# Kernel optimization log

Measured on AMD Instinct MI355X. Metric: run time of the kernel, lower is better.

The kernel has to match this reference:

```python
import jax, jax.numpy as jnp
import numpy as np

SEQ, BATCH, HIDDEN = 2048, 2, 1024
NUM_HEADS, HEAD_DIM = 16, 64
LN_EPS = 1e-6
NEG_INF = -1e10


def setup_inputs() -> dict:
    key = jax.random.key(0)
    k1, k2, k3 = jax.random.split(key, 3)
    inputs_q = jax.random.normal(k1, (SEQ, BATCH, HIDDEN), dtype=jnp.float32)
    ln_scale = jnp.ones((HIDDEN,), dtype=jnp.float32)
    ln_bias = jnp.zeros((HIDDEN,), dtype=jnp.float32)
    # fused QKV kernel: (hidden, 3, num_heads*head_dim), fan_in variance scaling
    qkv_kernel = jax.random.normal(k2, (HIDDEN, 3, NUM_HEADS * HEAD_DIM), dtype=jnp.float32) / np.sqrt(HIDDEN).astype(np.float32)
    out_kernel = jax.random.normal(k3, (NUM_HEADS * HEAD_DIM, HIDDEN), dtype=jnp.float32) / np.sqrt(NUM_HEADS * HEAD_DIM).astype(np.float32)
    return {"inputs_q": inputs_q, "ln_scale": ln_scale, "ln_bias": ln_bias,
            "qkv_kernel": qkv_kernel, "out_kernel": out_kernel}


def reference(inputs_q, ln_scale, ln_bias, qkv_kernel, out_kernel):
    s, b, h = inputs_q.shape
    # --- LayerNorm (fused with QKV projection in the original module) ---
    mu = jnp.mean(inputs_q, axis=-1, keepdims=True)
    var = jnp.mean(jnp.square(inputs_q - mu), axis=-1, keepdims=True)
    ln_out = (inputs_q - mu) * jax.lax.rsqrt(var + LN_EPS) * ln_scale + ln_bias
    # --- fused QKV projection: (s,b,h) @ (h,3,nh*hd) -> (s,b,3,nh*hd) ---
    qkv = jnp.einsum('sbh,htk->stbk', ln_out, qkv_kernel)  # (s,3,b,nh*hd)
    q = qkv[:, 0].reshape(s, b, NUM_HEADS, HEAD_DIM)  # (s,b,nh,hd)
    k = qkv[:, 1].reshape(s, b, NUM_HEADS, HEAD_DIM)
    v = qkv[:, 2].reshape(s, b, NUM_HEADS, HEAD_DIM)
    # --- core attention (transpose_batch_sequence=True layout) ---
    scale = 1.0 / np.sqrt(HEAD_DIM).astype(np.float32)  # scale_attn_logits=True
    logits = jnp.einsum('qbhd,kbhd->bhqk', q, k) * scale
    causal = jnp.tril(jnp.ones((s, s), dtype=bool))  # attn_mask_type='causal'
    logits = jnp.where(causal[None, None], logits, jnp.asarray(NEG_INF, logits.dtype))
    attn = jax.nn.softmax(logits, axis=-1)
    ctx = jnp.einsum('bhqk,kbhd->qbhd', attn, v).reshape(s, b, NUM_HEADS * HEAD_DIM)
    # --- output projection ---
    return jnp.einsum('sbk,kh->sbh', ctx, out_kernel)
```

## Files before the change

kernel.cpp:

```cpp
#include <hip/hip_runtime.h>

typedef unsigned short u16;
typedef unsigned int u32;
typedef __attribute__((ext_vector_type(8))) short short8;
typedef __attribute__((ext_vector_type(4))) float f32x4;

#define AS1C(p) ((const __attribute__((address_space(1))) void*)(p))
#define AS3(p)  ((__attribute__((address_space(3))) void*)(p))

constexpr int SEQ = 2048, BATCH = 2, HIDDEN = 1024, NH = 16, HD = 64;
constexpr int MROWS = SEQ * BATCH;
constexpr int QKV_N = 3 * NH * HD;
#define Q_SCALE 0.18033688011112042f

__device__ __forceinline__ float bf2f(u16 u) {
  union { u32 i; float f; } v; v.i = (u32)u << 16; return v.f;
}
__device__ __forceinline__ u16 f2bf(float f) {
  union { float f; u32 i; } v; v.f = f;
  u32 r = v.i + 0x7fffu + ((v.i >> 16) & 1u);
  return (u16)(r >> 16);
}
__device__ __forceinline__ u32 cvt_pk_bf16(float lo, float hi) {
  u32 r;
  asm("v_cvt_pk_bf16_f32 %0, %1, %2" : "=v"(r) : "v"(lo), "v"(hi));
  return r;
}
__device__ __forceinline__ bool is_f32(const unsigned* probe) { return probe[0] == 0x3F800000u; }

__global__ __launch_bounds__(256) void transpose_k(const void* __restrict__ in,
                                                   u16* __restrict__ out, int R, int C,
                                                   const unsigned* __restrict__ probe) {
  __shared__ alignas(16) u16 t[32][33];
  const bool fm = is_f32(probe);
  int c0 = blockIdx.x * 32, r0 = blockIdx.y * 32;
  int tx = threadIdx.x & 31, ty = threadIdx.x >> 5;
  if (fm) {
    const float* fin = (const float*)in;
#pragma unroll
    for (int i = 0; i < 32; i += 8) t[ty + i][tx] = f2bf(fin[(size_t)(r0 + ty + i) * C + c0 + tx]);
  } else {
    const u16* uin = (const u16*)in;
#pragma unroll
    for (int i = 0; i < 32; i += 8) t[ty + i][tx] = uin[(size_t)(r0 + ty + i) * C + c0 + tx];
  }
  __syncthreads();
#pragma unroll
  for (int i = 0; i < 32; i += 8) out[(size_t)(c0 + ty + i) * R + r0 + tx] = t[tx][ty + i];
}

__global__ __launch_bounds__(256) void ln_k(const void* __restrict__ xv, const void* __restrict__ gv,
                                            const void* __restrict__ bv, u16* __restrict__ y,
                                            const unsigned* __restrict__ probe) {
  const bool fm = is_f32(probe);
  int row = blockIdx.x, t = threadIdx.x;
  float f0, f1, f2, f3, g0, g1, g2, g3, b0, b1, b2, b3;
  if (fm) {
    float4 v = *(const float4*)((const float*)xv + (size_t)row * HIDDEN + t * 4);
    f0 = v.x; f1 = v.y; f2 = v.z; f3 = v.w;
    float4 gg = *(const float4*)((const float*)gv + t * 4);
    g0 = gg.x; g1 = gg.y; g2 = gg.z; g3 = gg.w;
    float4 bb = *(const float4*)((const float*)bv + t * 4);
    b0 = bb.x; b1 = bb.y; b2 = bb.z; b3 = bb.w;
  } else {
    ushort4 v = *(const ushort4*)((const u16*)xv + (size_t)row * HIDDEN + t * 4);
    f0 = bf2f(v.x); f1 = bf2f(v.y); f2 = bf2f(v.z); f3 = bf2f(v.w);
    ushort4 gg = *(const ushort4*)((const u16*)gv + t * 4);
    g0 = bf2f(gg.x); g1 = bf2f(gg.y); g2 = bf2f(gg.z); g3 = bf2f(gg.w);
    ushort4 bb = *(const ushort4*)((const u16*)bv + t * 4);
    b0 = bf2f(bb.x); b1 = bf2f(bb.y); b2 = bf2f(bb.z); b3 = bf2f(bb.w);
  }
  float s = f0 + f1 + f2 + f3;
  float s2 = f0 * f0 + f1 * f1 + f2 * f2 + f3 * f3;
#pragma unroll
  for (int off = 1; off < 64; off <<= 1) { s += __shfl_xor(s, off); s2 += __shfl_xor(s2, off); }
  __shared__ float ps[4], ps2[4];
  int w = t >> 6, lane = t & 63;
  if (lane == 0) { ps[w] = s; ps2[w] = s2; }
  __syncthreads();
  s = ps[0] + ps[1] + ps[2] + ps[3];
  s2 = ps2[0] + ps2[1] + ps2[2] + ps2[3];
  float mu = s * (1.0f / HIDDEN);
  float rstd = rsqrtf(s2 * (1.0f / HIDDEN) - mu * mu + 1e-6f);
  ushort4 o;
  o.x = f2bf((f0 - mu) * rstd * g0 + b0);
  o.y = f2bf((f1 - mu) * rstd * g1 + b1);
  o.z = f2bf((f2 - mu) * rstd * g2 + b2);
  o.w = f2bf((f3 - mu) * rstd * g3 + b3);
  *(ushort4*)(y + (size_t)row * HIDDEN + t * 4) = o;
}

template <int EPI>
__global__ __launch_bounds__(256) void gemm_k(const u16* __restrict__ A, const u16* __restrict__ Bt,
                                              void* __restrict__ o0, u16* __restrict__ o1,
                                              u16* __restrict__ o2, int M, int N, int K,
                                              const unsigned* __restrict__ probe) {
  __shared__ alignas(16) u16 As[128 * 32];
  __shared__ alignas(16) u16 Bs[128 * 32];
  const int bm = blockIdx.x, bn = blockIdx.y;
  const int tid = threadIdx.x, w = tid >> 6, lane = tid & 63;
  const int wr = w >> 1, wc = w & 1, lr = lane & 15, lk = lane >> 4;
  f32x4 acc[4][4] = {};

  const int srow_lo = lane >> 2;
  const int sslot = lane & 3;
  const int csw = ((lk ^ ((lr >> 1) & 3)) * 8);

  for (int k0 = 0; k0 < K; k0 += 32) {
#pragma unroll
    for (int j = 0; j < 2; j++) {
      const int issue = w * 2 + j;
      const int row = issue * 16 + srow_lo;
      const int src = ((sslot ^ ((row >> 1) & 3)) * 8);
      __builtin_amdgcn_global_load_lds(AS1C(A + (size_t)(bm * 128 + row) * K + k0 + src),
                                       AS3(As + issue * 512 + lane * 8), 16, 0, 0);
      __builtin_amdgcn_global_load_lds(AS1C(Bt + (size_t)(bn * 128 + row) * K + k0 + src),
                                       AS3(Bs + issue * 512 + lane * 8), 16, 0, 0);
    }
    __syncthreads();
    short8 a[4], b[4];
#pragma unroll
    for (int i = 0; i < 4; i++) {
      a[i] = *(const short8*)(As + (wr * 64 + i * 16 + lr) * 32 + csw);
      b[i] = *(const short8*)(Bs + (wc * 64 + i * 16 + lr) * 32 + csw);
    }
#pragma unroll
    for (int mi = 0; mi < 4; mi++)
#pragma unroll
      for (int ni = 0; ni < 4; ni++)
        acc[mi][ni] = __builtin_amdgcn_mfma_f32_16x16x32_bf16(a[mi], b[ni], acc[mi][ni], 0, 0, 0);
    __syncthreads();
  }

  const int r0 = bm * 128 + wr * 64, c0 = bn * 128 + wc * 64;
  if constexpr (EPI == 0) {
    const bool fm = is_f32(probe);
#pragma unroll
    for (int mi = 0; mi < 4; mi++)
#pragma unroll
      for (int ni = 0; ni < 4; ni++) {
        int col = c0 + ni * 16 + lr;
#pragma unroll
        for (int j = 0; j < 4; j++) {
          int row = r0 + mi * 16 + lk * 4 + j;
          if (fm) ((float*)o0)[(size_t)row * N + col] = acc[mi][ni][j];
          else    ((u16*)o0)[(size_t)row * N + col] = f2bf(acc[mi][ni][j]);
        }
      }
  } else {
#pragma unroll
    for (int mi = 0; mi < 4; mi++)
#pragma unroll
      for (int ni = 0; ni < 4; ni++) {
        int n = c0 + ni * 16 + lr;
        int t = n >> 10, rem = n & 1023, h = rem >> 6, d = rem & 63;
#pragma unroll
        for (int j = 0; j < 4; j++) {
          int r = r0 + mi * 16 + lk * 4 + j;
          int s = r >> 1, bb = r & 1;
          size_t bh = (size_t)(bb * NH + h);
          if (t == 0)      ((u16*)o0)[(bh * SEQ + s) * HD + d] = f2bf(acc[mi][ni][j] * Q_SCALE);
          else if (t == 1) o1[(bh * SEQ + s) * HD + d] = f2bf(acc[mi][ni][j]);
          else             o2[(bh * HD + d) * SEQ + s] = f2bf(acc[mi][ni][j]);
        }
      }
  }
}

__global__ __launch_bounds__(256, 3) void attn_k(const u16* __restrict__ Q, const u16* __restrict__ Kb,
                                                 const u16* __restrict__ VT, u16* __restrict__ ctx) {
  const int flat = blockIdx.x;
  const int xu = flat & 7, idx = flat >> 3;
  const int bh = xu * 4 + (idx & 3);
  const int qt = 31 - (idx >> 2);
  const int tid = threadIdx.x;
  const int w = tid >> 6, lane = tid & 63;
  const int lr = lane & 15, lk = lane >> 4;
  const size_t base = (size_t)bh * SEQ * HD;
  const int b = bh >> 4, h = bh & 15;

  __shared__ alignas(16) u16 Ks[2][4096];
  __shared__ alignas(16) u16 Vs[2][4096];
  __shared__ alignas(16) u16 P[4][16 * 72];
  u16* Pw = &P[w][0];
  u32* Pw32 = (u32*)Pw;

  const int st_r = lane >> 3;
  const int st_c = 8 * ((lane & 7) ^ st_r);

  const int qr0 = qt * 64 + w * 16;
  const int qrow = qr0 + lr;
  const int klast = qt;

  short8 aq[2];
#pragma unroll
  for (int kk = 0; kk < 2; kk++)
    aq[kk] = *(const short8*)(Q + base + (size_t)qrow * HD + kk * 32 + lk * 8);

  f32x4 o[4] = {};
  float m = -1e30f, l = 0.0f;

#pragma unroll
  for (int j = 0; j < 2; j++) {
    const int c = j * 4 + w;
    const int r = c * 8 + st_r;
    __builtin_amdgcn_global_load_lds(AS1C(Kb + base + (size_t)r * HD + st_c),
                                     AS3(Ks[0] + c * 512), 16, 0, 0);
    __builtin_amdgcn_global_load_lds(AS1C(VT + base + (size_t)r * SEQ + st_c),
                                     AS3(Vs[0] + c * 512), 16, 0, 0);
  }
  __syncthreads();

  for (int kt = 0; kt <= klast; kt++) {
    const int k0 = kt * 64;
    const int buf = kt & 1;
    if (kt < klast) {
      const int kn = k0 + 64;
#pragma unroll
      for (int j = 0; j < 2; j++) {
        const int c = j * 4 + w;
        const int r = c * 8 + st_r;
        __builtin_amdgcn_global_load_lds(AS1C(Kb + base + (size_t)(kn + r) * HD + st_c),
                                         AS3(Ks[buf ^ 1] + c * 512), 16, 0, 0);
        __builtin_amdgcn_global_load_lds(AS1C(VT + base + (size_t)r * SEQ + kn + st_c),
                                         AS3(Vs[buf ^ 1] + c * 512), 16, 0, 0);
      }
    }
    const int swz = (lr & 7) << 3;
    short8 bk[4][2], bv[4][2];
#pragma unroll
    for (int ni = 0; ni < 4; ni++) {
      const int row = ni * 16 + lr;
#pragma unroll
      for (int kk = 0; kk < 2; kk++)
        bk[ni][kk] = *(const short8*)(Ks[buf] + row * 64 + ((kk * 32 + lk * 8) ^ swz));
#pragma unroll
      for (int ks = 0; ks < 2; ks++)
        bv[ni][ks] = *(const short8*)(Vs[buf] + row * 64 + ((ks * 32 + lk * 8) ^ swz));
    }
    f32x4 s[4] = {};
    __builtin_amdgcn_s_setprio(1);
#pragma unroll
    for (int ni = 0; ni < 4; ni++)
#pragma unroll
      for (int kk = 0; kk < 2; kk++)
        s[ni] = __builtin_amdgcn_mfma_f32_16x16x32_bf16(bk[ni][kk], aq[kk], s[ni], 0, 0, 0);
    __builtin_amdgcn_s_setprio(0);
    if (kt == klast) {
#pragma unroll
      for (int ni = 0; ni < 4; ni++)
#pragma unroll
        for (int j = 0; j < 4; j++)
          if (k0 + ni * 16 + lk * 4 + j > qrow) s[ni][j] = -1e30f;
    }
    float pm = s[0][0];
#pragma unroll
    for (int ni = 0; ni < 4; ni++)
#pragma unroll
      for (int j = 0; j < 4; j++) pm = fmaxf(pm, s[ni][j]);
    pm = fmaxf(pm, __shfl_xor(pm, 16));
    pm = fmaxf(pm, __shfl_xor(pm, 32));
    const float nm = fmaxf(m, pm);
    const float fac = exp2f(m - nm);
    float rs = 0.0f;
#pragma unroll
    for (int ni = 0; ni < 4; ni++)
#pragma unroll
      for (int j = 0; j < 4; j++) {
        float p = exp2f(s[ni][j] - nm);
        s[ni][j] = p;
        rs += p;
      }
    rs += __shfl_xor(rs, 16);
    rs += __shfl_xor(rs, 32);
    l = l * fac + rs;
    m = nm;
#pragma unroll
    for (int ni = 0; ni < 4; ni++) {
      uint2 pk;
      pk.x = cvt_pk_bf16(s[ni][0], s[ni][1]);
      pk.y = cvt_pk_bf16(s[ni][2], s[ni][3]);
      *(uint2*)(Pw32 + lr * 36 + ni * 8 + lk * 2) = pk;
    }
    short8 pa[2];
#pragma unroll
    for (int kk = 0; kk < 2; kk++)
      pa[kk] = *(const short8*)(Pw + lr * 72 + kk * 32 + lk * 8);
    float f0 = __shfl(fac, lk * 4 + 0);
    float f1 = __shfl(fac, lk * 4 + 1);
    float f2 = __shfl(fac, lk * 4 + 2);
    float f3 = __shfl(fac, lk * 4 + 3);
#pragma unroll
    for (int ni = 0; ni < 4; ni++) {
      o[ni][0] *= f0; o[ni][1] *= f1; o[ni][2] *= f2; o[ni][3] *= f3;
    }
    __builtin_amdgcn_s_setprio(1);
#pragma unroll
    for (int ni = 0; ni < 4; ni++)
#pragma unroll
      for (int kk = 0; kk < 2; kk++)
        o[ni] = __builtin_amdgcn_mfma_f32_16x16x32_bf16(pa[kk], bv[ni][kk], o[ni], 0, 0, 0);
    __builtin_amdgcn_s_setprio(0);
    __syncthreads();
  }
  float linv0 = 1.0f / __shfl(l, lk * 4 + 0);
  float linv1 = 1.0f / __shfl(l, lk * 4 + 1);
  float linv2 = 1.0f / __shfl(l, lk * 4 + 2);
  float linv3 = 1.0f / __shfl(l, lk * 4 + 3);
#pragma unroll
  for (int ni = 0; ni < 4; ni++) {
    int col = h * HD + ni * 16 + lr;
    ctx[(size_t)((qr0 + lk * 4 + 0) * BATCH + b) * (NH * HD) + col] = f2bf(o[ni][0] * linv0);
    ctx[(size_t)((qr0 + lk * 4 + 1) * BATCH + b) * (NH * HD) + col] = f2bf(o[ni][1] * linv1);
    ctx[(size_t)((qr0 + lk * 4 + 2) * BATCH + b) * (NH * HD) + col] = f2bf(o[ni][2] * linv2);
    ctx[(size_t)((qr0 + lk * 4 + 3) * BATCH + b) * (NH * HD) + col] = f2bf(o[ni][3] * linv3);
  }
}

extern "C" void kernel_launch(void* const* d_in, const int* in_sizes, int n_in,
                              void* d_out, int out_size, void* d_ws, size_t ws_size,
                              hipStream_t stream) {
  const void* x    = d_in[0];
  const void* g    = d_in[1];
  const void* bta  = d_in[2];
  const void* wqkv = d_in[3];
  const void* wout = d_in[4];
  const unsigned* probe = (const unsigned*)d_in[1];

  char* ws = (char*)d_ws;
  u16* ln   = (u16*)(ws);
  u16* q    = (u16*)(ws + 8388608);
  u16* k    = (u16*)(ws + 16777216);
  u16* vT   = (u16*)(ws + 25165824);
  u16* qkvT = (u16*)(ws + 33554432);
  u16* outT = (u16*)(ws + 33554432 + 6291456);
  u16* ctx  = ln;

  transpose_k<<<dim3(QKV_N / 32, HIDDEN / 32), 256, 0, stream>>>(wqkv, qkvT, HIDDEN, QKV_N, probe);
  transpose_k<<<dim3(HIDDEN / 32, HIDDEN / 32), 256, 0, stream>>>(wout, outT, HIDDEN, HIDDEN, probe);
  ln_k<<<MROWS, 256, 0, stream>>>(x, g, bta, ln, probe);
  gemm_k<1><<<dim3(MROWS / 128, QKV_N / 128), 256, 0, stream>>>(ln, qkvT, q, k, vT,
                                                                MROWS, QKV_N, HIDDEN, probe);
  attn_k<<<dim3(1024), 256, 0, stream>>>(q, k, vT, ctx);
  gemm_k<0><<<dim3(MROWS / 128, HIDDEN / 128), 256, 0, stream>>>(ctx, outT, d_out, nullptr,
                                                                 nullptr, MROWS, HIDDEN,
                                                                 HIDDEN, probe);
}
```

Baseline: 134.9 us.

## Double-buffer GEMM LDS tiles and skip attention rescale when max is stable

The GEMM kernel now keeps two LDS buffers and issues the next k-tile's global-to-LDS loads before computing on the current one, which removes one barrier per iteration and overlaps memory traffic with MFMA work. The attention softmax uses a lazy rescale: the running max and the output/denominator rescale are updated only when some lane's new max exceeds the old one by more than 8 (in log2 units). The max and sum reductions are also rewritten as trees. The cost is twice the LDS for the GEMM tiles, and probabilities can reach up to 2^8 before bf16 packing, which bf16 range tolerates.

```diff
diff --git a/kernel.cpp b/kernel.cpp
--- a/kernel.cpp
+++ b/kernel.cpp
@@ -95,8 +95,8 @@
                                               void* __restrict__ o0, u16* __restrict__ o1,
                                               u16* __restrict__ o2, int M, int N, int K,
                                               const unsigned* __restrict__ probe) {
-  __shared__ alignas(16) u16 As[128 * 32];
-  __shared__ alignas(16) u16 Bs[128 * 32];
+  __shared__ alignas(16) u16 As[2][128 * 32];
+  __shared__ alignas(16) u16 Bs[2][128 * 32];
   const int bm = blockIdx.x, bn = blockIdx.y;
   const int tid = threadIdx.x, w = tid >> 6, lane = tid & 63;
   const int wr = w >> 1, wc = w & 1, lr = lane & 15, lk = lane >> 4;
@@ -105,24 +105,42 @@
   const int srow_lo = lane >> 2;
   const int sslot = lane & 3;
   const int csw = ((lk ^ ((lr >> 1) & 3)) * 8);
-
-  for (int k0 = 0; k0 < K; k0 += 32) {
-#pragma unroll
-    for (int j = 0; j < 2; j++) {
-      const int issue = w * 2 + j;
-      const int row = issue * 16 + srow_lo;
-      const int src = ((sslot ^ ((row >> 1) & 3)) * 8);
-      __builtin_amdgcn_global_load_lds(AS1C(A + (size_t)(bm * 128 + row) * K + k0 + src),
-                                       AS3(As + issue * 512 + lane * 8), 16, 0, 0);
-      __builtin_amdgcn_global_load_lds(AS1C(Bt + (size_t)(bn * 128 + row) * K + k0 + src),
-                                       AS3(Bs + issue * 512 + lane * 8), 16, 0, 0);
-    }
-    __syncthreads();
+  const int nk = K >> 5;
+
+  int srowA[2], srcA[2];
+#pragma unroll
+  for (int j = 0; j < 2; j++) {
+    const int issue = w * 2 + j;
+    srowA[j] = issue * 16 + srow_lo;
+    srcA[j] = ((sslot ^ ((srowA[j] >> 1) & 3)) * 8);
+  }
+
+#define STAGE(kt, bufi)                                                                     \
+  {                                                                                         \
+    const int k0s = (kt) * 32;                                                              \
+    _Pragma("unroll")                                                                       \
+    for (int j = 0; j < 2; j++) {                                                           \
+      const int issue = w * 2 + j;                                                          \
+      __builtin_amdgcn_global_load_lds(                                                     \
+          AS1C(A + (size_t)(bm * 128 + srowA[j]) * K + k0s + srcA[j]),                      \
+          AS3(As[bufi] + issue * 512 + lane * 8), 16, 0, 0);                                \
+      __builtin_amdgcn_global_load_lds(                                                     \
+          AS1C(Bt + (size_t)(bn * 128 + srowA[j]) * K + k0s + srcA[j]),                     \
+          AS3(Bs[bufi] + issue * 512 + lane * 8), 16, 0, 0);                                \
+    }                                                                                       \
+  }
+
+  STAGE(0, 0);
+  __syncthreads();
+
+  int buf = 0;
+  for (int kt = 0; kt < nk; ++kt) {
+    if (kt + 1 < nk) STAGE(kt + 1, buf ^ 1);
     short8 a[4], b[4];
 #pragma unroll
     for (int i = 0; i < 4; i++) {
-      a[i] = *(const short8*)(As + (wr * 64 + i * 16 + lr) * 32 + csw);
-      b[i] = *(const short8*)(Bs + (wc * 64 + i * 16 + lr) * 32 + csw);
+      a[i] = *(const short8*)(As[buf] + (wr * 64 + i * 16 + lr) * 32 + csw);
+      b[i] = *(const short8*)(Bs[buf] + (wc * 64 + i * 16 + lr) * 32 + csw);
     }
 #pragma unroll
     for (int mi = 0; mi < 4; mi++)
@@ -130,7 +148,9 @@
       for (int ni = 0; ni < 4; ni++)
         acc[mi][ni] = __builtin_amdgcn_mfma_f32_16x16x32_bf16(a[mi], b[ni], acc[mi][ni], 0, 0, 0);
     __syncthreads();
-  }
+    buf ^= 1;
+  }
+#undef STAGE
 
   const int r0 = bm * 128 + wr * 64, c0 = bn * 128 + wc * 64;
   if constexpr (EPI == 0) {
@@ -253,28 +273,38 @@
         for (int j = 0; j < 4; j++)
           if (k0 + ni * 16 + lk * 4 + j > qrow) s[ni][j] = -1e30f;
     }
-    float pm = s[0][0];
+    float pmn[4];
 #pragma unroll
     for (int ni = 0; ni < 4; ni++)
-#pragma unroll
-      for (int j = 0; j < 4; j++) pm = fmaxf(pm, s[ni][j]);
+      pmn[ni] = fmaxf(fmaxf(s[ni][0], s[ni][1]), fmaxf(s[ni][2], s[ni][3]));
+    float pm = fmaxf(fmaxf(pmn[0], pmn[1]), fmaxf(pmn[2], pmn[3]));
     pm = fmaxf(pm, __shfl_xor(pm, 16));
     pm = fmaxf(pm, __shfl_xor(pm, 32));
-    const float nm = fmaxf(m, pm);
-    const float fac = exp2f(m - nm);
-    float rs = 0.0f;
-#pragma unroll
-    for (int ni = 0; ni < 4; ni++)
-#pragma unroll
-      for (int j = 0; j < 4; j++) {
-        float p = exp2f(s[ni][j] - nm);
-        s[ni][j] = p;
-        rs += p;
+    if (!__all(pm - m <= 8.0f)) {
+      const float nm = fmaxf(m, pm);
+      const float fac = exp2f(m - nm);
+      m = nm;
+      l *= fac;
+      float f0 = __shfl(fac, lk * 4 + 0);
+      float f1 = __shfl(fac, lk * 4 + 1);
+      float f2 = __shfl(fac, lk * 4 + 2);
+      float f3 = __shfl(fac, lk * 4 + 3);
+#pragma unroll
+      for (int ni = 0; ni < 4; ni++) {
+        o[ni][0] *= f0; o[ni][1] *= f1; o[ni][2] *= f2; o[ni][3] *= f3;
       }
+    }
+    float rsn[4];
+#pragma unroll
+    for (int ni = 0; ni < 4; ni++) {
+#pragma unroll
+      for (int j = 0; j < 4; j++) s[ni][j] = exp2f(s[ni][j] - m);
+      rsn[ni] = (s[ni][0] + s[ni][1]) + (s[ni][2] + s[ni][3]);
+    }
+    float rs = (rsn[0] + rsn[1]) + (rsn[2] + rsn[3]);
     rs += __shfl_xor(rs, 16);
     rs += __shfl_xor(rs, 32);
-    l = l * fac + rs;
-    m = nm;
+    l += rs;
 #pragma unroll
     for (int ni = 0; ni < 4; ni++) {
       uint2 pk;
@@ -286,14 +316,6 @@
 #pragma unroll
     for (int kk = 0; kk < 2; kk++)
       pa[kk] = *(const short8*)(Pw + lr * 72 + kk * 32 + lk * 8);
-    float f0 = __shfl(fac, lk * 4 + 0);
-    float f1 = __shfl(fac, lk * 4 + 1);
-    float f2 = __shfl(fac, lk * 4 + 2);
-    float f3 = __shfl(fac, lk * 4 + 3);
-#pragma unroll
-    for (int ni = 0; ni < 4; ni++) {
-      o[ni][0] *= f0; o[ni][1] *= f1; o[ni][2] *= f2; o[ni][3] *= f3;
-    }
     __builtin_amdgcn_s_setprio(1);
 #pragma unroll
     for (int ni = 0; ni < 4; ni++)
```

Result: faster. 122.8 us (-8.9%).
